# Optimization experiments

Hardware: AMD Instinct MI355X
Metric: run time of the kernel (lower is better)

The kernel has to match this reference:

```python
import jax, jax.numpy as jnp
import numpy as np

B, LQ, LKV, D, DV = 8, 2048, 2048, 128, 128


def setup_inputs() -> dict:
    key = jax.random.key(0)
    kq, kk, kv = jax.random.split(key, 3)
    return {
        "query": jax.random.normal(kq, (B, LQ, D), dtype=jnp.float32),
        "key": jax.random.normal(kk, (B, LKV, D), dtype=jnp.float32),
        "value": jax.random.normal(kv, (B, LKV, DV), dtype=jnp.float32),
    }


def reference(query, key, value):
    # score_fn: scaled dot-product  score = Q K^T / sqrt(Dq)
    scale = 1.0 / jnp.sqrt(jnp.asarray(query.shape[-1], query.dtype))
    score = jnp.einsum("bqd,bkd->bqk", query, key) * scale  # (B, Lq, Lkv)
    attention_weights = jax.nn.softmax(score, axis=-1)
    context_vector = jnp.einsum("bqk,bkv->bqv", attention_weights, value)
    return attention_weights, context_vector
```

## Files before the change

kernel.cpp:

```cpp
#include <hip/hip_runtime.h>

#define BB    8
#define LQN   2048
#define LKVN  2048
#define DQ    128
#define DVN   128
#define QT    32
#define KVW   32
#define KTI   128
#define NT    (LKVN / KTI)
#define OSTR  132

typedef short short8 __attribute__((ext_vector_type(8)));
typedef float f32x4  __attribute__((ext_vector_type(4)));
typedef int   int4v  __attribute__((ext_vector_type(4)));

__device__ __forceinline__ short f2bf(float f) {
  unsigned u = __builtin_bit_cast(unsigned, f);
  u += 0x7fffu + ((u >> 16) & 1u);
  return (short)(u >> 16);
}

__device__ __forceinline__ int packbf(float a, float b) {
  unsigned lo = (unsigned short)f2bf(a);
  unsigned hi = (unsigned short)f2bf(b);
  return (int)(lo | (hi << 16));
}

__global__ __launch_bounds__(256) void pre_kernel(const float* __restrict__ K,
                                                  const float* __restrict__ V,
                                                  short* __restrict__ Kb,
                                                  short* __restrict__ Vt) {
  __shared__ float tile[128][33];
  if (blockIdx.x >= 512) {
    int i = (blockIdx.x - 512) * 256 + threadIdx.x;
    size_t off = (size_t)i * 8;
    float4 a = *(const float4*)(K + off);
    float4 c = *(const float4*)(K + off + 4);
    short8 o;
    o[0] = f2bf(a.x); o[1] = f2bf(a.y); o[2] = f2bf(a.z); o[3] = f2bf(a.w);
    o[4] = f2bf(c.x); o[5] = f2bf(c.y); o[6] = f2bf(c.z); o[7] = f2bf(c.w);
    *(short8*)(Kb + off) = o;
    return;
  }
  const int bx  = blockIdx.x;
  const int kv0 = (bx & 15) * 128;
  const int dv0 = ((bx >> 4) & 3) * 32;
  const int b   = bx >> 6;
  const int tid = threadIdx.x;
  const float* src = V + ((size_t)b * LKVN + kv0) * DVN + dv0;
#pragma unroll
  for (int it = 0; it < 4; ++it) {
    int idx = it * 256 + tid;
    int r = idx >> 3, c4 = idx & 7;
    float4 v = *(const float4*)(src + (size_t)r * DVN + c4 * 4);
    tile[r][c4 * 4 + 0] = v.x;
    tile[r][c4 * 4 + 1] = v.y;
    tile[r][c4 * 4 + 2] = v.z;
    tile[r][c4 * 4 + 3] = v.w;
  }
  __syncthreads();
  short* dst = Vt + ((size_t)b * DVN + dv0) * LKVN + kv0;
#pragma unroll
  for (int it = 0; it < 2; ++it) {
    int idx = it * 256 + tid;
    int row = idx >> 4, ch = idx & 15;
    short8 o;
#pragma unroll
    for (int j = 0; j < 8; ++j) o[j] = f2bf(tile[ch * 8 + j][row]);
    *(short8*)(dst + (size_t)row * LKVN + ch * 8) = o;
  }
}

#define P1_BODY(kc, kn, t)                                                          \
  {                                                                                 \
    if ((t) + 1 < NT) {                                                             \
      _Pragma("unroll")                                                             \
      for (int t2 = 0; t2 < 2; ++t2)                                                \
        _Pragma("unroll")                                                           \
        for (int ks = 0; ks < 4; ++ks)                                              \
          kn[t2 * 4 + ks] =                                                         \
              *(const short8*)(Kw + ((size_t)(((t) + 1) * KTI + t2 * 16)) * DQ + ks * 32); \
    }                                                                               \
    _Pragma("unroll")                                                               \
    for (int g = 0; g < 2; ++g)                                                     \
      _Pragma("unroll")                                                             \
      for (int t2 = 0; t2 < 2; ++t2) {                                              \
        f32x4 acc = {0.f, 0.f, 0.f, 0.f};                                           \
        _Pragma("unroll")                                                           \
        for (int ks = 0; ks < 4; ++ks)                                              \
          acc = __builtin_amdgcn_mfma_f32_16x16x32_bf16(kc[t2 * 4 + ks], qf[g][ks], acc, 0, 0, 0); \
        _Pragma("unroll")                                                           \
        for (int r = 0; r < 4; ++r) l_part[g] += __expf(acc[r] * scale);            \
      }                                                                             \
  }

#define P2_BODY(t)                                                                  \
  {                                                                                 \
    _Pragma("unroll")                                                               \
    for (int t2 = 0; t2 < 2; ++t2)                                                  \
      _Pragma("unroll")                                                             \
      for (int ks = 0; ks < 4; ++ks)                                                \
        kA[t2 * 4 + ks] =                                                           \
            *(const short8*)(Kw + ((size_t)((t) * KTI + t2 * 16)) * DQ + ks * 32);  \
    short8 vf[8];                                                                   \
    _Pragma("unroll")                                                               \
    for (int dvg = 0; dvg < 8; ++dvg)                                               \
      vf[dvg] = *(const short8*)(Vw + (size_t)(dvg * 16) * LKVN + (t) * KTI);       \
    int pk[2][2][2];                                                                \
    _Pragma("unroll")                                                               \
    for (int g = 0; g < 2; ++g)                                                     \
      _Pragma("unroll")                                                             \
      for (int t2 = 0; t2 < 2; ++t2) {                                              \
        f32x4 acc = {0.f, 0.f, 0.f, 0.f};                                           \
        _Pragma("unroll")                                                           \
        for (int ks = 0; ks < 4; ++ks)                                              \
          acc = __builtin_amdgcn_mfma_f32_16x16x32_bf16(kA[t2 * 4 + ks], qf[g][ks], acc, 0, 0, 0); \
        float p0 = __expf(acc[0] * scale) * rinv[g];                                \
        float p1 = __expf(acc[1] * scale) * rinv[g];                                \
        float p2 = __expf(acc[2] * scale) * rinv[g];                                \
        float p3 = __expf(acc[3] * scale) * rinv[g];                                \
        f32x4 st = {p0, p1, p2, p3};                                                \
        *(f32x4*)(Wrow + (size_t)(g * 16) * LKVN + (t) * KTI + t2 * 16) = st;       \
        pk[g][t2][0] = packbf(p0, p1);                                              \
        pk[g][t2][1] = packbf(p2, p3);                                              \
      }                                                                             \
    _Pragma("unroll")                                                               \
    for (int g = 0; g < 2; ++g) {                                                   \
      int a0 = __shfl(pk[g][0][0], srcA, 64);                                       \
      int b0 = __shfl(pk[g][1][0], srcA, 64);                                       \
      int a1 = __shfl(pk[g][0][1], srcA, 64);                                       \
      int b1 = __shfl(pk[g][1][1], srcA, 64);                                       \
      int a2 = __shfl(pk[g][0][0], srcB, 64);                                       \
      int b2 = __shfl(pk[g][1][0], srcB, 64);                                       \
      int a3 = __shfl(pk[g][0][1], srcB, 64);                                       \
      int b3 = __shfl(pk[g][1][1], srcB, 64);                                       \
      int4v bi;                                                                     \
      bi[0] = sel ? b0 : a0;                                                        \
      bi[1] = sel ? b1 : a1;                                                        \
      bi[2] = sel ? b2 : a2;                                                        \
      bi[3] = sel ? b3 : a3;                                                        \
      short8 bfr = __builtin_bit_cast(short8, bi);                                  \
      _Pragma("unroll")                                                             \
      for (int dvg = 0; dvg < 8; ++dvg)                                             \
        oacc[g][dvg] = __builtin_amdgcn_mfma_f32_16x16x32_bf16(vf[dvg], bfr, oacc[g][dvg], 0, 0, 0); \
    }                                                                               \
  }

__global__ __launch_bounds__(256, 2) void attn_kernel(const float* __restrict__ Q,
                                                      const short* __restrict__ Kb,
                                                      const short* __restrict__ Vt,
                                                      float* __restrict__ W,
                                                      float* __restrict__ O) {
  __shared__ __align__(16) float osum[2][QT][OSTR];
  __shared__ float red_l[4][QT];

  const int tid  = threadIdx.x;
  const int w    = tid >> 6;
  const int lane = tid & 63;
  const int n    = lane & 15;
  const int qd   = lane >> 4;
  const int b    = blockIdx.x & 7;
  const int q0   = (blockIdx.x >> 3) * QT;

  const short* Kw = Kb + ((size_t)b * LKVN + w * KVW + n) * DQ + qd * 8;
  const short* Vw = Vt + ((size_t)b * DVN + n) * LKVN + w * KVW + qd * 8;
  float* Wrow = W + ((size_t)b * LQN + q0 + n) * LKVN + w * KVW + qd * 4;

  short8 qf[2][4];
#pragma unroll
  for (int g = 0; g < 2; ++g) {
    const float* Qrow = Q + ((size_t)b * LQN + q0 + g * 16 + n) * DQ + qd * 8;
#pragma unroll
    for (int ks = 0; ks < 4; ++ks) {
      float4 f0 = *(const float4*)(Qrow + ks * 32);
      float4 f1 = *(const float4*)(Qrow + ks * 32 + 4);
      short8 o;
      o[0] = f2bf(f0.x); o[1] = f2bf(f0.y); o[2] = f2bf(f0.z); o[3] = f2bf(f0.w);
      o[4] = f2bf(f1.x); o[5] = f2bf(f1.y); o[6] = f2bf(f1.z); o[7] = f2bf(f1.w);
      qf[g][ks] = o;
    }
  }

  const float scale = 0.08838834764831845f;
  float l_part[2] = {0.f, 0.f};

  short8 kA[8], kB[8];
#pragma unroll
  for (int t2 = 0; t2 < 2; ++t2)
#pragma unroll
    for (int ks = 0; ks < 4; ++ks)
      kA[t2 * 4 + ks] = *(const short8*)(Kw + ((size_t)(t2 * 16)) * DQ + ks * 32);

  for (int t = 0; t < NT; t += 2) {
    P1_BODY(kA, kB, t)
    P1_BODY(kB, kA, t + 1)
  }

#pragma unroll
  for (int g = 0; g < 2; ++g) {
    l_part[g] += __shfl_xor(l_part[g], 16, 64);
    l_part[g] += __shfl_xor(l_part[g], 32, 64);
  }
  if (lane < 16) {
    red_l[w][lane]      = l_part[0];
    red_l[w][16 + lane] = l_part[1];
  }
  __syncthreads();
  float rinv[2];
#pragma unroll
  for (int g = 0; g < 2; ++g) {
    int qq = g * 16 + n;
    rinv[g] = 1.0f / (red_l[0][qq] + red_l[1][qq] + red_l[2][qq] + red_l[3][qq]);
  }

  const int srcA = n + ((qd & 1) << 5);
  const int srcB = srcA + 16;
  const int sel  = qd >> 1;

  f32x4 oacc[2][8];
#pragma unroll
  for (int g = 0; g < 2; ++g)
#pragma unroll
    for (int dvg = 0; dvg < 8; ++dvg) oacc[g][dvg] = (f32x4){0.f, 0.f, 0.f, 0.f};

  for (int t = 0; t < NT; ++t) {
    P2_BODY(t)
  }

  if (w < 2) {
#pragma unroll
    for (int g = 0; g < 2; ++g)
#pragma unroll
      for (int dvg = 0; dvg < 8; ++dvg)
        *(f32x4*)&osum[w][g * 16 + n][dvg * 16 + qd * 4] = oacc[g][dvg];
  }
  __syncthreads();
  if (w >= 2) {
#pragma unroll
    for (int g = 0; g < 2; ++g)
#pragma unroll
      for (int dvg = 0; dvg < 8; ++dvg) {
        f32x4* p = (f32x4*)&osum[w - 2][g * 16 + n][dvg * 16 + qd * 4];
        *p = *p + oacc[g][dvg];
      }
  }
  __syncthreads();

  float* Ob = O + ((size_t)b * LQN + q0) * DVN;
  const int qq = tid >> 3;
  const int c0 = (tid & 7) * 16;
#pragma unroll
  for (int c = 0; c < 4; ++c) {
    f32x4 s = *(const f32x4*)&osum[0][qq][c0 + c * 4];
    f32x4 s1 = *(const f32x4*)&osum[1][qq][c0 + c * 4];
    s = s + s1;
    *(f32x4*)(Ob + (size_t)qq * DVN + c0 + c * 4) = s;
  }
}

extern "C" void kernel_launch(void* const* d_in, const int* in_sizes, int n_in,
                              void* d_out, int out_size, void* d_ws, size_t ws_size,
                              hipStream_t stream) {
  const float* Q = (const float*)d_in[0];
  const float* K = (const float*)d_in[1];
  const float* V = (const float*)d_in[2];
  float* W = (float*)d_out;
  float* O = W + (size_t)BB * LQN * LKVN;
  short* Kb = (short*)d_ws;
  short* Vt = Kb + (size_t)BB * LKVN * DQ;

  pre_kernel<<<1536, 256, 0, stream>>>(K, V, Kb, Vt);
  attn_kernel<<<512, 256, 0, stream>>>(Q, Kb, Vt, W, O);
}
```

Before: 233.5 us.

## Halve query tile to 16 rows, double grid, raise occupancy, add MFMA priority hints

The query tile per block shrinks from 32 to 16 rows, so each wave holds one Q fragment group and one output accumulator set. Launch bounds go to 4 blocks per CU and the grid doubles to 1024 blocks. The second pass is inlined with explicit prefetch of the next K tile and s_setprio around the MFMA groups, aiming for better latency hiding through higher occupancy. In exchange, every K/V tile is now loaded and converted twice as often per query row, which doubles K/V read traffic, and the QK^T work is still repeated across both passes.

```diff
diff --git a/kernel.cpp b/kernel.cpp
--- a/kernel.cpp
+++ b/kernel.cpp
@@ -5,7 +5,7 @@
 #define LKVN  2048
 #define DQ    128
 #define DVN   128
-#define QT    32
+#define QT    16
 #define KVW   32
 #define KTI   128
 #define NT    (LKVN / KTI)
@@ -83,71 +83,17 @@
               *(const short8*)(Kw + ((size_t)(((t) + 1) * KTI + t2 * 16)) * DQ + ks * 32); \
     }                                                                               \
     _Pragma("unroll")                                                               \
-    for (int g = 0; g < 2; ++g)                                                     \
-      _Pragma("unroll")                                                             \
-      for (int t2 = 0; t2 < 2; ++t2) {                                              \
-        f32x4 acc = {0.f, 0.f, 0.f, 0.f};                                           \
-        _Pragma("unroll")                                                           \
-        for (int ks = 0; ks < 4; ++ks)                                              \
-          acc = __builtin_amdgcn_mfma_f32_16x16x32_bf16(kc[t2 * 4 + ks], qf[g][ks], acc, 0, 0, 0); \
-        _Pragma("unroll")                                                           \
-        for (int r = 0; r < 4; ++r) l_part[g] += __expf(acc[r] * scale);            \
-      }                                                                             \
-  }
-
-#define P2_BODY(t)                                                                  \
-  {                                                                                 \
-    _Pragma("unroll")                                                               \
-    for (int t2 = 0; t2 < 2; ++t2)                                                  \
+    for (int t2 = 0; t2 < 2; ++t2) {                                                \
+      f32x4 acc = {0.f, 0.f, 0.f, 0.f};                                             \
       _Pragma("unroll")                                                             \
       for (int ks = 0; ks < 4; ++ks)                                                \
-        kA[t2 * 4 + ks] =                                                           \
-            *(const short8*)(Kw + ((size_t)((t) * KTI + t2 * 16)) * DQ + ks * 32);  \
-    short8 vf[8];                                                                   \
-    _Pragma("unroll")                                                               \
-    for (int dvg = 0; dvg < 8; ++dvg)                                               \
-      vf[dvg] = *(const short8*)(Vw + (size_t)(dvg * 16) * LKVN + (t) * KTI);       \
-    int pk[2][2][2];                                                                \
-    _Pragma("unroll")                                                               \
-    for (int g = 0; g < 2; ++g)                                                     \
+        acc = __builtin_amdgcn_mfma_f32_16x16x32_bf16(kc[t2 * 4 + ks], qf[ks], acc, 0, 0, 0); \
       _Pragma("unroll")                                                             \
-      for (int t2 = 0; t2 < 2; ++t2) {                                              \
-        f32x4 acc = {0.f, 0.f, 0.f, 0.f};                                           \
-        _Pragma("unroll")                                                           \
-        for (int ks = 0; ks < 4; ++ks)                                              \
-          acc = __builtin_amdgcn_mfma_f32_16x16x32_bf16(kA[t2 * 4 + ks], qf[g][ks], acc, 0, 0, 0); \
-        float p0 = __expf(acc[0] * scale) * rinv[g];                                \
-        float p1 = __expf(acc[1] * scale) * rinv[g];                                \
-        float p2 = __expf(acc[2] * scale) * rinv[g];                                \
-        float p3 = __expf(acc[3] * scale) * rinv[g];                                \
-        f32x4 st = {p0, p1, p2, p3};                                                \
-        *(f32x4*)(Wrow + (size_t)(g * 16) * LKVN + (t) * KTI + t2 * 16) = st;       \
-        pk[g][t2][0] = packbf(p0, p1);                                              \
-        pk[g][t2][1] = packbf(p2, p3);                                              \
-      }                                                                             \
-    _Pragma("unroll")                                                               \
-    for (int g = 0; g < 2; ++g) {                                                   \
-      int a0 = __shfl(pk[g][0][0], srcA, 64);                                       \
-      int b0 = __shfl(pk[g][1][0], srcA, 64);                                       \
-      int a1 = __shfl(pk[g][0][1], srcA, 64);                                       \
-      int b1 = __shfl(pk[g][1][1], srcA, 64);                                       \
-      int a2 = __shfl(pk[g][0][0], srcB, 64);                                       \
-      int b2 = __shfl(pk[g][1][0], srcB, 64);                                       \
-      int a3 = __shfl(pk[g][0][1], srcB, 64);                                       \
-      int b3 = __shfl(pk[g][1][1], srcB, 64);                                       \
-      int4v bi;                                                                     \
-      bi[0] = sel ? b0 : a0;                                                        \
-      bi[1] = sel ? b1 : a1;                                                        \
-      bi[2] = sel ? b2 : a2;                                                        \
-      bi[3] = sel ? b3 : a3;                                                        \
-      short8 bfr = __builtin_bit_cast(short8, bi);                                  \
-      _Pragma("unroll")                                                             \
-      for (int dvg = 0; dvg < 8; ++dvg)                                             \
-        oacc[g][dvg] = __builtin_amdgcn_mfma_f32_16x16x32_bf16(vf[dvg], bfr, oacc[g][dvg], 0, 0, 0); \
+      for (int r = 0; r < 4; ++r) l_part += __expf(acc[r] * scale);                 \
     }                                                                               \
   }
 
-__global__ __launch_bounds__(256, 2) void attn_kernel(const float* __restrict__ Q,
+__global__ __launch_bounds__(256, 4) void attn_kernel(const float* __restrict__ Q,
                                                       const short* __restrict__ Kb,
                                                       const short* __restrict__ Vt,
                                                       float* __restrict__ W,
@@ -167,10 +113,9 @@
   const short* Vw = Vt + ((size_t)b * DVN + n) * LKVN + w * KVW + qd * 8;
   float* Wrow = W + ((size_t)b * LQN + q0 + n) * LKVN + w * KVW + qd * 4;
 
-  short8 qf[2][4];
-#pragma unroll
-  for (int g = 0; g < 2; ++g) {
-    const float* Qrow = Q + ((size_t)b * LQN + q0 + g * 16 + n) * DQ + qd * 8;
+  short8 qf[4];
+  {
+    const float* Qrow = Q + ((size_t)b * LQN + q0 + n) * DQ + qd * 8;
 #pragma unroll
     for (int ks = 0; ks < 4; ++ks) {
       float4 f0 = *(const float4*)(Qrow + ks * 32);
@@ -178,12 +123,12 @@
       short8 o;
       o[0] = f2bf(f0.x); o[1] = f2bf(f0.y); o[2] = f2bf(f0.z); o[3] = f2bf(f0.w);
       o[4] = f2bf(f1.x); o[5] = f2bf(f1.y); o[6] = f2bf(f1.z); o[7] = f2bf(f1.w);
-      qf[g][ks] = o;
+      qf[ks] = o;
     }
   }
 
   const float scale = 0.08838834764831845f;
-  float l_part[2] = {0.f, 0.f};
+  float l_part = 0.f;
 
   short8 kA[8], kB[8];
 #pragma unroll
@@ -197,65 +142,109 @@
     P1_BODY(kB, kA, t + 1)
   }
 
-#pragma unroll
-  for (int g = 0; g < 2; ++g) {
-    l_part[g] += __shfl_xor(l_part[g], 16, 64);
-    l_part[g] += __shfl_xor(l_part[g], 32, 64);
-  }
-  if (lane < 16) {
-    red_l[w][lane]      = l_part[0];
-    red_l[w][16 + lane] = l_part[1];
-  }
-  __syncthreads();
-  float rinv[2];
-#pragma unroll
-  for (int g = 0; g < 2; ++g) {
-    int qq = g * 16 + n;
-    rinv[g] = 1.0f / (red_l[0][qq] + red_l[1][qq] + red_l[2][qq] + red_l[3][qq]);
-  }
+  l_part += __shfl_xor(l_part, 16, 64);
+  l_part += __shfl_xor(l_part, 32, 64);
+  if (lane < 16) red_l[w][lane] = l_part;
+  __syncthreads();
+  const float rinv = 1.0f / (red_l[0][n] + red_l[1][n] + red_l[2][n] + red_l[3][n]);
 
   const int srcA = n + ((qd & 1) << 5);
   const int srcB = srcA + 16;
   const int sel  = qd >> 1;
 
-  f32x4 oacc[2][8];
-#pragma unroll
-  for (int g = 0; g < 2; ++g)
-#pragma unroll
-    for (int dvg = 0; dvg < 8; ++dvg) oacc[g][dvg] = (f32x4){0.f, 0.f, 0.f, 0.f};
+  f32x4 oacc[8];
+#pragma unroll
+  for (int dvg = 0; dvg < 8; ++dvg) oacc[dvg] = (f32x4){0.f, 0.f, 0.f, 0.f};
+
+#pragma unroll
+  for (int t2 = 0; t2 < 2; ++t2)
+#pragma unroll
+    for (int ks = 0; ks < 4; ++ks)
+      kA[t2 * 4 + ks] = *(const short8*)(Kw + ((size_t)(t2 * 16)) * DQ + ks * 32);
 
   for (int t = 0; t < NT; ++t) {
-    P2_BODY(t)
+    f32x4 acc[2];
+    __builtin_amdgcn_s_setprio(1);
+#pragma unroll
+    for (int t2 = 0; t2 < 2; ++t2) {
+      acc[t2] = (f32x4){0.f, 0.f, 0.f, 0.f};
+#pragma unroll
+      for (int ks = 0; ks < 4; ++ks)
+        acc[t2] = __builtin_amdgcn_mfma_f32_16x16x32_bf16(kA[t2 * 4 + ks], qf[ks], acc[t2], 0, 0, 0);
+    }
+    __builtin_amdgcn_s_setprio(0);
+
+    if (t + 1 < NT) {
+#pragma unroll
+      for (int t2 = 0; t2 < 2; ++t2)
+#pragma unroll
+        for (int ks = 0; ks < 4; ++ks)
+          kA[t2 * 4 + ks] =
+              *(const short8*)(Kw + ((size_t)((t + 1) * KTI + t2 * 16)) * DQ + ks * 32);
+    }
+    short8 vf[8];
+#pragma unroll
+    for (int dvg = 0; dvg < 8; ++dvg)
+      vf[dvg] = *(const short8*)(Vw + (size_t)(dvg * 16) * LKVN + t * KTI);
+
+    int pk[2][2];
+#pragma unroll
+    for (int t2 = 0; t2 < 2; ++t2) {
+      float p0 = __expf(acc[t2][0] * scale) * rinv;
+      float p1 = __expf(acc[t2][1] * scale) * rinv;
+      float p2 = __expf(acc[t2][2] * scale) * rinv;
+      float p3 = __expf(acc[t2][3] * scale) * rinv;
+      f32x4 st = {p0, p1, p2, p3};
+      *(f32x4*)(Wrow + t * KTI + t2 * 16) = st;
+      pk[t2][0] = packbf(p0, p1);
+      pk[t2][1] = packbf(p2, p3);
+    }
+    int a0 = __shfl(pk[0][0], srcA, 64);
+    int b0 = __shfl(pk[1][0], srcA, 64);
+    int a1 = __shfl(pk[0][1], srcA, 64);
+    int b1 = __shfl(pk[1][1], srcA, 64);
+    int a2 = __shfl(pk[0][0], srcB, 64);
+    int b2 = __shfl(pk[1][0], srcB, 64);
+    int a3 = __shfl(pk[0][1], srcB, 64);
+    int b3 = __shfl(pk[1][1], srcB, 64);
+    int4v bi;
+    bi[0] = sel ? b0 : a0;
+    bi[1] = sel ? b1 : a1;
+    bi[2] = sel ? b2 : a2;
+    bi[3] = sel ? b3 : a3;
+    short8 bfr = __builtin_bit_cast(short8, bi);
+
+    __builtin_amdgcn_s_setprio(1);
+#pragma unroll
+    for (int dvg = 0; dvg < 8; ++dvg)
+      oacc[dvg] = __builtin_amdgcn_mfma_f32_16x16x32_bf16(vf[dvg], bfr, oacc[dvg], 0, 0, 0);
+    __builtin_amdgcn_s_setprio(0);
   }
 
   if (w < 2) {
 #pragma unroll
-    for (int g = 0; g < 2; ++g)
-#pragma unroll
-      for (int dvg = 0; dvg < 8; ++dvg)
-        *(f32x4*)&osum[w][g * 16 + n][dvg * 16 + qd * 4] = oacc[g][dvg];
+    for (int dvg = 0; dvg < 8; ++dvg)
+      *(f32x4*)&osum[w][n][dvg * 16 + qd * 4] = oacc[dvg];
   }
   __syncthreads();
   if (w >= 2) {
 #pragma unroll
-    for (int g = 0; g < 2; ++g)
-#pragma unroll
-      for (int dvg = 0; dvg < 8; ++dvg) {
-        f32x4* p = (f32x4*)&osum[w - 2][g * 16 + n][dvg * 16 + qd * 4];
-        *p = *p + oacc[g][dvg];
-      }
+    for (int dvg = 0; dvg < 8; ++dvg) {
+      f32x4* p = (f32x4*)&osum[w - 2][n][dvg * 16 + qd * 4];
+      *p = *p + oacc[dvg];
+    }
   }
   __syncthreads();
 
   float* Ob = O + ((size_t)b * LQN + q0) * DVN;
-  const int qq = tid >> 3;
-  const int c0 = (tid & 7) * 16;
-#pragma unroll
-  for (int c = 0; c < 4; ++c) {
-    f32x4 s = *(const f32x4*)&osum[0][qq][c0 + c * 4];
+  const int qq = tid >> 4;
+  const int c0 = (tid & 15) * 8;
+#pragma unroll
+  for (int c = 0; c < 2; ++c) {
+    f32x4 s0 = *(const f32x4*)&osum[0][qq][c0 + c * 4];
     f32x4 s1 = *(const f32x4*)&osum[1][qq][c0 + c * 4];
-    s = s + s1;
-    *(f32x4*)(Ob + (size_t)qq * DVN + c0 + c * 4) = s;
+    s0 = s0 + s1;
+    *(f32x4*)(Ob + (size_t)qq * DVN + c0 + c * 4) = s0;
   }
 }
 
@@ -271,5 +260,5 @@
   short* Vt = Kb + (size_t)BB * LKVN * DQ;
 
   pre_kernel<<<1536, 256, 0, stream>>>(K, V, Kb, Vt);
-  attn_kernel<<<512, 256, 0, stream>>>(Q, Kb, Vt, W, O);
-}
+  attn_kernel<<<1024, 256, 0, stream>>>(Q, Kb, Vt, W, O);
+}
```

After: 336.1 us. +44.0%, slower.
